# Kernel tuning notes

Measured on AMD Instinct MI355X. Metric: run time of the kernel, lower is better.

Reference implementation:

```python
import jax, jax.numpy as jnp
import numpy as np

DECAY = 0.99
EPS = 1e-5
NUM_EMBEDDINGS = 8192


def setup_inputs() -> dict:
    key = jax.random.key(0)
    k1, k2 = jax.random.split(key)
    N, D, K = 65536, 64, NUM_EMBEDDINGS
    x = jax.random.normal(k1, (N, D), dtype=jnp.float32)
    vq_embedding = jax.random.uniform(k2, (K, D), dtype=jnp.float32)
    vq_cluster_size = jnp.ones((K,), dtype=jnp.float32)
    return {"x": x, "vq_embedding": vq_embedding, "vq_cluster_size": vq_cluster_size}


def reference(x, vq_embedding, vq_cluster_size):
    N, D = x.shape
    K = vq_embedding.shape[0]

    # BatchNorm1d(affine=False), training mode: normalize with batch stats (biased var)
    mean = jnp.mean(x, axis=0)                      # [D]
    var = jnp.var(x, axis=0)                        # biased, [D]
    xn = (x - mean) / jnp.sqrt(var + EPS)           # [N, D]

    # pairwise squared distances [N, K]
    distances = (jnp.sum(xn * xn, axis=1, keepdims=True)
                 + jnp.sum(vq_embedding * vq_embedding, axis=1)
                 - 2.0 * (xn @ vq_embedding.T))
    idx = jnp.argmin(distances, axis=1)             # [N]

    # one-hot scatter expressed as segment sums
    dw = jax.ops.segment_sum(xn, idx, num_segments=K)                      # [K, D]
    counts = jax.ops.segment_sum(jnp.ones((N,), x.dtype), idx, num_segments=K)  # [K]

    # EMA codebook update
    new_emb = vq_cluster_size[:, None] * vq_embedding * DECAY + (1.0 - DECAY) * dw
    new_size = vq_cluster_size * DECAY + (1.0 - DECAY) * counts
    new_emb = new_emb / new_size[:, None]

    # BN running stats with momentum=None (cumulative avg, first batch):
    # running_mean = batch mean, running_var = unbiased batch var
    unbiased_var = var * (N / (N - 1))
    running_std = jnp.sqrt(unbiased_var + EPS)
    vq_embedding_output = new_emb * running_std[None, :] + mean[None, :]

    return vq_embedding_output, new_emb, new_size
```

## Files before the change

### kernel.cpp

```cpp
#include <hip/hip_runtime.h>

#define NROWS 65536
#define DIM 64
#define KCODES 8192
#define DECAYF 0.99f
#define EPSV 1e-5f
#define KD (KCODES * DIM)
#define KSPLIT 4
#define KC (KCODES / KSPLIT)
#define ROUNDS (KC / 128)

typedef _Float16 half8 __attribute__((ext_vector_type(8)));
typedef float f32x16 __attribute__((ext_vector_type(16)));

#define WS_STATS  0
#define WS_NHCK   256
#define WS_EBUF   8448
#define WS_PSUM   270592
#define WS_PSQ    286976
#define WS_PACKED 303360
#define WS_DW     368896
#define WS_COUNTS 893184
#define ZERO_F4   149504

__global__ __launch_bounds__(256) void k_prep_stats(
    const float* __restrict__ emb, const float* __restrict__ x,
    half8* __restrict__ ebuf, float* __restrict__ nhck,
    float* __restrict__ psum, float* __restrict__ psq,
    float4* __restrict__ zbase)
{
    const int tid = blockIdx.x * 256 + threadIdx.x;

    #pragma unroll
    for (int i = 0; i < 3; ++i) {
        int z = tid + i * 65536;
        if (z < ZERO_F4) zbase[z] = float4{0.f, 0.f, 0.f, 0.f};
    }

    {
        const int code = tid >> 3, sub = tid & 7;
        const int c = sub >> 1, h = sub & 1;
        const float* e = emb + (size_t)code * DIM + c * 16 + h * 8;
        float4 a = *(const float4*)e;
        float4 b = *(const float4*)(e + 4);
        float f[8] = {a.x, a.y, a.z, a.w, b.x, b.y, b.z, b.w};
        half8 hh;
        float ssq = 0.f;
        #pragma unroll
        for (int i = 0; i < 8; ++i) {
            hh[i] = (_Float16)(f[i] - 0.5f);
            ssq += f[i] * f[i];
        }
        #pragma unroll
        for (int o = 1; o < 8; o <<= 1) ssq += __shfl_xor(ssq, o, 64);
        if (sub == 0) nhck[code] = 10.6875f - 0.5f * ssq;
        const int R = code >> 7, t = (code >> 5) & 3, col = code & 31;
        ebuf[(size_t)R * 1024 + t * 256 + c * 64 + h * 32 + col] = hh;
    }

    {
        const int wave = threadIdx.x >> 6;
        const int col  = threadIdx.x & 63;
        const int base = blockIdx.x * 256;
        float s = 0.f, q = 0.f;
        #pragma unroll 4
        for (int i = 0; i < 64; ++i) {
            int r = base + i * 4 + wave;
            float v = x[(size_t)r * DIM + col];
            s += v;
            q += v * v;
        }
        __shared__ float ls[4][64];
        __shared__ float lq[4][64];
        ls[wave][col] = s;
        lq[wave][col] = q;
        __syncthreads();
        if (threadIdx.x < 64) {
            psum[blockIdx.x * 64 + col] = ls[0][col] + ls[1][col] + ls[2][col] + ls[3][col];
            psq[blockIdx.x * 64 + col]  = lq[0][col] + lq[1][col] + lq[2][col] + lq[3][col];
        }
    }
}

__global__ __launch_bounds__(256) void k_colstats_final(
    const float* __restrict__ psum, const float* __restrict__ psq,
    float* __restrict__ stats)
{
    const int col = threadIdx.x & 63, part = threadIdx.x >> 6;
    float s = 0.f, q = 0.f;
    for (int i = part * 64; i < part * 64 + 64; ++i) {
        s += psum[i * 64 + col];
        q += psq[i * 64 + col];
    }
    __shared__ float ls[4][64];
    __shared__ float lq[4][64];
    ls[part][col] = s;
    lq[part][col] = q;
    __syncthreads();
    if (threadIdx.x < 64) {
        s = ls[0][col] + ls[1][col] + ls[2][col] + ls[3][col];
        q = lq[0][col] + lq[1][col] + lq[2][col] + lq[3][col];
        const float n = (float)NROWS;
        float mean = s / n;
        float var = q / n - mean * mean;
        if (var < 0.f) var = 0.f;
        stats[col]       = mean;
        stats[64 + col]  = 1.0f / sqrtf(var + EPSV);
        stats[128 + col] = sqrtf(var * (n / (n - 1.0f)) + EPSV);
    }
}

__device__ __forceinline__ void gload16(const void* g, void* l)
{
    __builtin_amdgcn_global_load_lds(
        (const __attribute__((address_space(1))) void*)g,
        (__attribute__((address_space(3))) void*)l, 16, 0, 0);
}

__global__ __launch_bounds__(256) void k_argmin32(
    const float* __restrict__ x, const half8* __restrict__ ebuf,
    const float* __restrict__ nhckg, const float* __restrict__ stats,
    unsigned* __restrict__ packed)
{
    __shared__ half8 smem[2048];

    const int lane = threadIdx.x & 63;
    const int wave = threadIdx.x >> 6;
    const int kc = blockIdx.y;
    const int col = lane & 31, h = lane >> 5;
    const int myrow = blockIdx.x * 128 + wave * 32 + col;

    half8 ah[4];
    {
        const float* xr = x + (size_t)myrow * DIM + h * 8;
        #pragma unroll
        for (int c = 0; c < 4; ++c) {
            float4 v0  = *(const float4*)(xr + c * 16);
            float4 v1  = *(const float4*)(xr + c * 16 + 4);
            float4 mu0 = *(const float4*)(stats + h * 8 + c * 16);
            float4 mu1 = *(const float4*)(stats + h * 8 + c * 16 + 4);
            float4 sg0 = *(const float4*)(stats + 64 + h * 8 + c * 16);
            float4 sg1 = *(const float4*)(stats + 64 + h * 8 + c * 16 + 4);
            ah[c][0] = (_Float16)((v0.x - mu0.x) * sg0.x);
            ah[c][1] = (_Float16)((v0.y - mu0.y) * sg0.y);
            ah[c][2] = (_Float16)((v0.z - mu0.z) * sg0.z);
            ah[c][3] = (_Float16)((v0.w - mu0.w) * sg0.w);
            ah[c][4] = (_Float16)((v1.x - mu1.x) * sg1.x);
            ah[c][5] = (_Float16)((v1.y - mu1.y) * sg1.y);
            ah[c][6] = (_Float16)((v1.z - mu1.z) * sg1.z);
            ah[c][7] = (_Float16)((v1.w - mu1.w) * sg1.w);
        }
    }

    float best[16];
    #pragma unroll
    for (int i = 0; i < 16; ++i) best[i] = -3.4e38f;

    const half8* esrc = ebuf + (size_t)kc * (KC * 8);
    const float* ckb = nhckg + kc * KC;

    {
        const char* src = (const char*)esrc + threadIdx.x * 16;
        char* dst = (char*)smem + threadIdx.x * 16;
        #pragma unroll
        for (int i = 0; i < 4; ++i) gload16(src + i * 4096, dst + i * 4096);
    }
    float nhck[4];
    #pragma unroll
    for (int t = 0; t < 4; ++t) nhck[t] = ckb[t * 32 + col];
    __syncthreads();

    for (int R = 0; R < ROUNDS; ++R) {
        const int buf = R & 1;
        float nhck_n[4] = {0.f, 0.f, 0.f, 0.f};
        if (R < ROUNDS - 1) {
            const char* src = (const char*)esrc + (size_t)(R + 1) * 16384 + threadIdx.x * 16;
            char* dst = (char*)smem + (buf ^ 1) * 16384 + threadIdx.x * 16;
            #pragma unroll
            for (int i = 0; i < 4; ++i) gload16(src + i * 4096, dst + i * 4096);
            #pragma unroll
            for (int t = 0; t < 4; ++t) nhck_n[t] = ckb[(R + 1) * 128 + t * 32 + col];
        }

        const half8* sb = smem + buf * 1024 + lane;
        #pragma unroll
        for (int t = 0; t < 4; ++t) {
            half8 b0 = sb[t * 256];
            half8 b1 = sb[t * 256 + 64];
            half8 b2 = sb[t * 256 + 128];
            half8 b3 = sb[t * 256 + 192];
            f32x16 acc;
            #pragma unroll
            for (int i = 0; i < 16; ++i) acc[i] = nhck[t];
            __builtin_amdgcn_s_setprio(1);
            acc = __builtin_amdgcn_mfma_f32_32x32x16_f16(ah[0], b0, acc, 0, 0, 0);
            acc = __builtin_amdgcn_mfma_f32_32x32x16_f16(ah[1], b1, acc, 0, 0, 0);
            acc = __builtin_amdgcn_mfma_f32_32x32x16_f16(ah[2], b2, acc, 0, 0, 0);
            acc = __builtin_amdgcn_mfma_f32_32x32x16_f16(ah[3], b3, acc, 0, 0, 0);
            __builtin_amdgcn_s_setprio(0);
            const unsigned key =
                (unsigned)(8191 - (kc * KC + R * 128 + t * 32 + col)) & 0x1FFFu;
            #pragma unroll
            for (int i = 0; i < 16; ++i) {
                unsigned u = (__float_as_uint(acc[i]) & 0xFFFFE000u) | key;
                best[i] = fmaxf(best[i], __uint_as_float(u));
            }
        }
        __syncthreads();
        #pragma unroll
        for (int t = 0; t < 4; ++t) nhck[t] = nhck_n[t];
    }

    #pragma unroll
    for (int off = 1; off < 32; off <<= 1) {
        #pragma unroll
        for (int i = 0; i < 16; ++i)
            best[i] = fmaxf(best[i], __shfl_xor(best[i], off, 64));
    }
    if (col == 0) {
        const int rbase = blockIdx.x * 128 + wave * 32 + 4 * h;
        #pragma unroll
        for (int i = 0; i < 16; ++i) {
            int row = rbase + (i & 3) + 8 * (i >> 2);
            unsigned u = __float_as_uint(best[i]);
            u = (u & 0x80000000u) ? ~u : (u | 0x80000000u);
            atomicMax(&packed[row], u);
        }
    }
}

__global__ __launch_bounds__(256) void k_scatter(
    const float* __restrict__ x, const float* __restrict__ stats,
    const unsigned* __restrict__ packed,
    float* __restrict__ dw, float* __restrict__ counts)
{
    const int t = blockIdx.x * 256 + threadIdx.x;
    const int row = t >> 6, col = t & 63;
    const unsigned v = packed[row];
    const unsigned key = (v & 0x80000000u) ? (v & 8191u) : (~v & 8191u);
    const int j = 8191 - (int)key;
    float xv = (x[(size_t)row * DIM + col] - stats[col]) * stats[64 + col];
    atomicAdd(&dw[(size_t)j * DIM + col], xv);
    if (col == 0) atomicAdd(&counts[j], 1.0f);
}

__global__ __launch_bounds__(256) void k_final(
    const float* __restrict__ emb, const float* __restrict__ cs,
    const float* __restrict__ dw, const float* __restrict__ counts,
    const float* __restrict__ stats, float* __restrict__ out)
{
    const int t = blockIdx.x * 256 + threadIdx.x;
    const int k = t >> 6, d = t & 63;
    float csk = cs[k];
    float ns = csk * DECAYF + (1.f - DECAYF) * counts[k];
    float ne = (csk * emb[t] * DECAYF + (1.f - DECAYF) * dw[t]) / ns;
    out[KD + t] = ne;
    out[t] = ne * stats[128 + d] + stats[d];
    if (d == 0) out[2 * KD + k] = ns;
}

extern "C" void kernel_launch(void* const* d_in, const int* in_sizes, int n_in,
                              void* d_out, int out_size, void* d_ws, size_t ws_size,
                              hipStream_t stream)
{
    const float* x   = (const float*)d_in[0];
    const float* emb = (const float*)d_in[1];
    const float* cs  = (const float*)d_in[2];
    float* out = (float*)d_out;
    float* ws  = (float*)d_ws;

    float* stats  = ws + WS_STATS;
    float* nhck   = ws + WS_NHCK;
    half8* ebuf   = (half8*)(ws + WS_EBUF);
    float* psum   = ws + WS_PSUM;
    float* psq    = ws + WS_PSQ;
    unsigned* packed = (unsigned*)(ws + WS_PACKED);
    float* dw     = ws + WS_DW;
    float* counts = ws + WS_COUNTS;

    k_prep_stats<<<256, 256, 0, stream>>>(emb, x, ebuf, nhck, psum, psq,
                                          (float4*)(ws + WS_PACKED));
    k_colstats_final<<<1, 256, 0, stream>>>(psum, psq, stats);
    dim3 g3(NROWS / 128, KSPLIT);
    k_argmin32<<<g3, 256, 0, stream>>>(x, ebuf, nhck, stats, packed);
    k_scatter<<<(NROWS * DIM) / 256, 256, 0, stream>>>(x, stats, packed, dw, counts);
    k_final<<<KD / 256, 256, 0, stream>>>(emb, cs, dw, counts, stats, out);
}
```

Measured before the change: 175.2 us.

## Switch argmin GEMM to 16x16x32 MFMA with XOR-swizzled codebook layout

Replaces the 32x32x16 MFMA tiling in the distance/argmin kernel with 16x16x32 MFMAs. Each wave now handles 16 rows instead of 32, the grid doubles in rows, and the codebook is repacked in LDS with an XOR swizzle to avoid bank conflicts. This shrinks per-thread accumulator and best-value registers (16 down to 4), aiming for higher occupancy and a cheaper epilogue. In exchange, each row block rereads the codebook twice as often and more LDS loads are issued per MFMA.

```diff
diff --git a/kernel.cpp b/kernel.cpp
--- a/kernel.cpp
+++ b/kernel.cpp
@@ -11,7 +11,7 @@
 #define ROUNDS (KC / 128)
 
 typedef _Float16 half8 __attribute__((ext_vector_type(8)));
-typedef float f32x16 __attribute__((ext_vector_type(16)));
+typedef float f32x4 __attribute__((ext_vector_type(4)));
 
 #define WS_STATS  0
 #define WS_NHCK   256
@@ -38,9 +38,8 @@
     }
 
     {
-        const int code = tid >> 3, sub = tid & 7;
-        const int c = sub >> 1, h = sub & 1;
-        const float* e = emb + (size_t)code * DIM + c * 16 + h * 8;
+        const int code = tid >> 3, ch = tid & 7;
+        const float* e = emb + (size_t)code * DIM + ch * 8;
         float4 a = *(const float4*)e;
         float4 b = *(const float4*)(e + 4);
         float f[8] = {a.x, a.y, a.z, a.w, b.x, b.y, b.z, b.w};
@@ -53,9 +52,9 @@
         }
         #pragma unroll
         for (int o = 1; o < 8; o <<= 1) ssq += __shfl_xor(ssq, o, 64);
-        if (sub == 0) nhck[code] = 10.6875f - 0.5f * ssq;
-        const int R = code >> 7, t = (code >> 5) & 3, col = code & 31;
-        ebuf[(size_t)R * 1024 + t * 256 + c * 64 + h * 32 + col] = hh;
+        if (ch == 0) nhck[code] = 10.6875f - 0.5f * ssq;
+        const int c = code & 15;
+        ebuf[(size_t)(code >> 4) * 128 + c * 8 + (ch ^ (c & 7))] = hh;
     }
 
     {
@@ -117,7 +116,7 @@
         (__attribute__((address_space(3))) void*)l, 16, 0, 0);
 }
 
-__global__ __launch_bounds__(256) void k_argmin32(
+__global__ __launch_bounds__(256) void k_argmin16(
     const float* __restrict__ x, const half8* __restrict__ ebuf,
     const float* __restrict__ nhckg, const float* __restrict__ stats,
     unsigned* __restrict__ packed)
@@ -127,37 +126,52 @@
     const int lane = threadIdx.x & 63;
     const int wave = threadIdx.x >> 6;
     const int kc = blockIdx.y;
-    const int col = lane & 31, h = lane >> 5;
-    const int myrow = blockIdx.x * 128 + wave * 32 + col;
-
-    half8 ah[4];
-    {
-        const float* xr = x + (size_t)myrow * DIM + h * 8;
-        #pragma unroll
-        for (int c = 0; c < 4; ++c) {
-            float4 v0  = *(const float4*)(xr + c * 16);
-            float4 v1  = *(const float4*)(xr + c * 16 + 4);
-            float4 mu0 = *(const float4*)(stats + h * 8 + c * 16);
-            float4 mu1 = *(const float4*)(stats + h * 8 + c * 16 + 4);
-            float4 sg0 = *(const float4*)(stats + 64 + h * 8 + c * 16);
-            float4 sg1 = *(const float4*)(stats + 64 + h * 8 + c * 16 + 4);
-            ah[c][0] = (_Float16)((v0.x - mu0.x) * sg0.x);
-            ah[c][1] = (_Float16)((v0.y - mu0.y) * sg0.y);
-            ah[c][2] = (_Float16)((v0.z - mu0.z) * sg0.z);
-            ah[c][3] = (_Float16)((v0.w - mu0.w) * sg0.w);
-            ah[c][4] = (_Float16)((v1.x - mu1.x) * sg1.x);
-            ah[c][5] = (_Float16)((v1.y - mu1.y) * sg1.y);
-            ah[c][6] = (_Float16)((v1.z - mu1.z) * sg1.z);
-            ah[c][7] = (_Float16)((v1.w - mu1.w) * sg1.w);
-        }
-    }
-
-    float best[16];
-    #pragma unroll
-    for (int i = 0; i < 16; ++i) best[i] = -3.4e38f;
+    const int c  = lane & 15;
+    const int kg = lane >> 4;
+    const int rowbase = blockIdx.x * 64 + wave * 16;
+    const int myrow = rowbase + c;
+
+    half8 a0, a1;
+    {
+        const float* xr = x + (size_t)myrow * DIM;
+        const int d0 = kg * 8, d1 = 32 + kg * 8;
+        float4 v0 = *(const float4*)(xr + d0);
+        float4 v1 = *(const float4*)(xr + d0 + 4);
+        float4 w0 = *(const float4*)(xr + d1);
+        float4 w1 = *(const float4*)(xr + d1 + 4);
+        float4 m0 = *(const float4*)(stats + d0);
+        float4 m1 = *(const float4*)(stats + d0 + 4);
+        float4 n0 = *(const float4*)(stats + d1);
+        float4 n1 = *(const float4*)(stats + d1 + 4);
+        float4 s0 = *(const float4*)(stats + 64 + d0);
+        float4 s1 = *(const float4*)(stats + 64 + d0 + 4);
+        float4 t0 = *(const float4*)(stats + 64 + d1);
+        float4 t1 = *(const float4*)(stats + 64 + d1 + 4);
+        a0[0] = (_Float16)((v0.x - m0.x) * s0.x);
+        a0[1] = (_Float16)((v0.y - m0.y) * s0.y);
+        a0[2] = (_Float16)((v0.z - m0.z) * s0.z);
+        a0[3] = (_Float16)((v0.w - m0.w) * s0.w);
+        a0[4] = (_Float16)((v1.x - m1.x) * s1.x);
+        a0[5] = (_Float16)((v1.y - m1.y) * s1.y);
+        a0[6] = (_Float16)((v1.z - m1.z) * s1.z);
+        a0[7] = (_Float16)((v1.w - m1.w) * s1.w);
+        a1[0] = (_Float16)((w0.x - n0.x) * t0.x);
+        a1[1] = (_Float16)((w0.y - n0.y) * t0.y);
+        a1[2] = (_Float16)((w0.z - n0.z) * t0.z);
+        a1[3] = (_Float16)((w0.w - n0.w) * t0.w);
+        a1[4] = (_Float16)((w1.x - n1.x) * t1.x);
+        a1[5] = (_Float16)((w1.y - n1.y) * t1.y);
+        a1[6] = (_Float16)((w1.z - n1.z) * t1.z);
+        a1[7] = (_Float16)((w1.w - n1.w) * t1.w);
+    }
+
+    float best[4];
+    #pragma unroll
+    for (int i = 0; i < 4; ++i) best[i] = -3.4e38f;
 
     const half8* esrc = ebuf + (size_t)kc * (KC * 8);
     const float* ckb = nhckg + kc * KC;
+    const unsigned kbase = (unsigned)(8191 - kc * KC - c);
 
     {
         const char* src = (const char*)esrc + threadIdx.x * 16;
@@ -165,63 +179,58 @@
         #pragma unroll
         for (int i = 0; i < 4; ++i) gload16(src + i * 4096, dst + i * 4096);
     }
-    float nhck[4];
-    #pragma unroll
-    for (int t = 0; t < 4; ++t) nhck[t] = ckb[t * 32 + col];
+    float nv[8];
+    #pragma unroll
+    for (int t = 0; t < 8; ++t) nv[t] = ckb[t * 16 + c];
     __syncthreads();
 
     for (int R = 0; R < ROUNDS; ++R) {
         const int buf = R & 1;
-        float nhck_n[4] = {0.f, 0.f, 0.f, 0.f};
+        float nvn[8] = {0.f, 0.f, 0.f, 0.f, 0.f, 0.f, 0.f, 0.f};
         if (R < ROUNDS - 1) {
             const char* src = (const char*)esrc + (size_t)(R + 1) * 16384 + threadIdx.x * 16;
             char* dst = (char*)smem + (buf ^ 1) * 16384 + threadIdx.x * 16;
             #pragma unroll
             for (int i = 0; i < 4; ++i) gload16(src + i * 4096, dst + i * 4096);
             #pragma unroll
-            for (int t = 0; t < 4; ++t) nhck_n[t] = ckb[(R + 1) * 128 + t * 32 + col];
-        }
-
-        const half8* sb = smem + buf * 1024 + lane;
-        #pragma unroll
-        for (int t = 0; t < 4; ++t) {
-            half8 b0 = sb[t * 256];
-            half8 b1 = sb[t * 256 + 64];
-            half8 b2 = sb[t * 256 + 128];
-            half8 b3 = sb[t * 256 + 192];
-            f32x16 acc;
-            #pragma unroll
-            for (int i = 0; i < 16; ++i) acc[i] = nhck[t];
+            for (int t = 0; t < 8; ++t) nvn[t] = ckb[(R + 1) * 128 + t * 16 + c];
+        }
+
+        const unsigned kR = kbase - (unsigned)(R * 128);
+        const half8* sb = smem + buf * 1024 + c * 8;
+        #pragma unroll
+        for (int t = 0; t < 8; ++t) {
+            half8 b0 = sb[t * 128 + (kg ^ (c & 7))];
+            half8 b1 = sb[t * 128 + ((kg + 4) ^ (c & 7))];
+            f32x4 acc;
+            #pragma unroll
+            for (int i = 0; i < 4; ++i) acc[i] = nv[t];
             __builtin_amdgcn_s_setprio(1);
-            acc = __builtin_amdgcn_mfma_f32_32x32x16_f16(ah[0], b0, acc, 0, 0, 0);
-            acc = __builtin_amdgcn_mfma_f32_32x32x16_f16(ah[1], b1, acc, 0, 0, 0);
-            acc = __builtin_amdgcn_mfma_f32_32x32x16_f16(ah[2], b2, acc, 0, 0, 0);
-            acc = __builtin_amdgcn_mfma_f32_32x32x16_f16(ah[3], b3, acc, 0, 0, 0);
+            acc = __builtin_amdgcn_mfma_f32_16x16x32_f16(a0, b0, acc, 0, 0, 0);
+            acc = __builtin_amdgcn_mfma_f32_16x16x32_f16(a1, b1, acc, 0, 0, 0);
             __builtin_amdgcn_s_setprio(0);
-            const unsigned key =
-                (unsigned)(8191 - (kc * KC + R * 128 + t * 32 + col)) & 0x1FFFu;
-            #pragma unroll
-            for (int i = 0; i < 16; ++i) {
+            const unsigned key = kR - (unsigned)(t * 16);
+            #pragma unroll
+            for (int i = 0; i < 4; ++i) {
                 unsigned u = (__float_as_uint(acc[i]) & 0xFFFFE000u) | key;
                 best[i] = fmaxf(best[i], __uint_as_float(u));
             }
         }
         __syncthreads();
         #pragma unroll
-        for (int t = 0; t < 4; ++t) nhck[t] = nhck_n[t];
-    }
-
-    #pragma unroll
-    for (int off = 1; off < 32; off <<= 1) {
-        #pragma unroll
-        for (int i = 0; i < 16; ++i)
+        for (int t = 0; t < 8; ++t) nv[t] = nvn[t];
+    }
+
+    #pragma unroll
+    for (int off = 1; off < 16; off <<= 1) {
+        #pragma unroll
+        for (int i = 0; i < 4; ++i)
             best[i] = fmaxf(best[i], __shfl_xor(best[i], off, 64));
     }
-    if (col == 0) {
-        const int rbase = blockIdx.x * 128 + wave * 32 + 4 * h;
-        #pragma unroll
-        for (int i = 0; i < 16; ++i) {
-            int row = rbase + (i & 3) + 8 * (i >> 2);
+    if (c == 0) {
+        #pragma unroll
+        for (int i = 0; i < 4; ++i) {
+            int row = rowbase + kg * 4 + i;
             unsigned u = __float_as_uint(best[i]);
             u = (u & 0x80000000u) ? ~u : (u | 0x80000000u);
             atomicMax(&packed[row], u);
@@ -281,8 +290,8 @@
     k_prep_stats<<<256, 256, 0, stream>>>(emb, x, ebuf, nhck, psum, psq,
                                           (float4*)(ws + WS_PACKED));
     k_colstats_final<<<1, 256, 0, stream>>>(psum, psq, stats);
-    dim3 g3(NROWS / 128, KSPLIT);
-    k_argmin32<<<g3, 256, 0, stream>>>(x, ebuf, nhck, stats, packed);
+    dim3 g3(NROWS / 64, KSPLIT);
+    k_argmin16<<<g3, 256, 0, stream>>>(x, ebuf, nhck, stats, packed);
     k_scatter<<<(NROWS * DIM) / 256, 256, 0, stream>>>(x, stats, packed, dw, counts);
     k_final<<<KD / 256, 256, 0, stream>>>(emb, cs, dw, counts, stats, out);
 }
```

After: 170.9 us. 2.5% less time.

## Process two 32-row A tiles per wave to reuse codebook fragments

Applied to the files above, without the earlier changes.

Each wave now handles 64 rows instead of 32, keeping two A-fragment sets and two accumulators so every B fragment read from LDS feeds two MFMA chains. The grid is halved in the row dimension. This halves the codebook LDS traffic and global staging per row and interleaves independent MFMAs to hide their latency. The cost is higher register pressure and fewer blocks (1024 total), which could lower occupancy.

```diff
diff --git a/kernel.cpp b/kernel.cpp
--- a/kernel.cpp
+++ b/kernel.cpp
@@ -117,6 +117,30 @@
         (__attribute__((address_space(3))) void*)l, 16, 0, 0);
 }
 
+__device__ __forceinline__ void build_afrag(const float* __restrict__ xr,
+                                            const float* __restrict__ stats,
+                                            int h, half8* a)
+{
+    #pragma unroll
+    for (int c = 0; c < 4; ++c) {
+        const int d = c * 16 + h * 8;
+        float4 v0 = *(const float4*)(xr + d);
+        float4 v1 = *(const float4*)(xr + d + 4);
+        float4 m0 = *(const float4*)(stats + d);
+        float4 m1 = *(const float4*)(stats + d + 4);
+        float4 s0 = *(const float4*)(stats + 64 + d);
+        float4 s1 = *(const float4*)(stats + 64 + d + 4);
+        a[c][0] = (_Float16)((v0.x - m0.x) * s0.x);
+        a[c][1] = (_Float16)((v0.y - m0.y) * s0.y);
+        a[c][2] = (_Float16)((v0.z - m0.z) * s0.z);
+        a[c][3] = (_Float16)((v0.w - m0.w) * s0.w);
+        a[c][4] = (_Float16)((v1.x - m1.x) * s1.x);
+        a[c][5] = (_Float16)((v1.y - m1.y) * s1.y);
+        a[c][6] = (_Float16)((v1.z - m1.z) * s1.z);
+        a[c][7] = (_Float16)((v1.w - m1.w) * s1.w);
+    }
+}
+
 __global__ __launch_bounds__(256) void k_argmin32(
     const float* __restrict__ x, const half8* __restrict__ ebuf,
     const float* __restrict__ nhckg, const float* __restrict__ stats,
@@ -128,33 +152,15 @@
     const int wave = threadIdx.x >> 6;
     const int kc = blockIdx.y;
     const int col = lane & 31, h = lane >> 5;
-    const int myrow = blockIdx.x * 128 + wave * 32 + col;
-
-    half8 ah[4];
-    {
-        const float* xr = x + (size_t)myrow * DIM + h * 8;
-        #pragma unroll
-        for (int c = 0; c < 4; ++c) {
-            float4 v0  = *(const float4*)(xr + c * 16);
-            float4 v1  = *(const float4*)(xr + c * 16 + 4);
-            float4 mu0 = *(const float4*)(stats + h * 8 + c * 16);
-            float4 mu1 = *(const float4*)(stats + h * 8 + c * 16 + 4);
-            float4 sg0 = *(const float4*)(stats + 64 + h * 8 + c * 16);
-            float4 sg1 = *(const float4*)(stats + 64 + h * 8 + c * 16 + 4);
-            ah[c][0] = (_Float16)((v0.x - mu0.x) * sg0.x);
-            ah[c][1] = (_Float16)((v0.y - mu0.y) * sg0.y);
-            ah[c][2] = (_Float16)((v0.z - mu0.z) * sg0.z);
-            ah[c][3] = (_Float16)((v0.w - mu0.w) * sg0.w);
-            ah[c][4] = (_Float16)((v1.x - mu1.x) * sg1.x);
-            ah[c][5] = (_Float16)((v1.y - mu1.y) * sg1.y);
-            ah[c][6] = (_Float16)((v1.z - mu1.z) * sg1.z);
-            ah[c][7] = (_Float16)((v1.w - mu1.w) * sg1.w);
-        }
-    }
-
-    float best[16];
-    #pragma unroll
-    for (int i = 0; i < 16; ++i) best[i] = -3.4e38f;
+    const int rowbase = blockIdx.x * 256 + wave * 64;
+
+    half8 a0[4], a1[4];
+    build_afrag(x + (size_t)(rowbase + col) * DIM, stats, h, a0);
+    build_afrag(x + (size_t)(rowbase + 32 + col) * DIM, stats, h, a1);
+
+    float best0[16], best1[16];
+    #pragma unroll
+    for (int i = 0; i < 16; ++i) { best0[i] = -3.4e38f; best1[i] = -3.4e38f; }
 
     const half8* esrc = ebuf + (size_t)kc * (KC * 8);
     const float* ckb = nhckg + kc * KC;
@@ -165,21 +171,21 @@
         #pragma unroll
         for (int i = 0; i < 4; ++i) gload16(src + i * 4096, dst + i * 4096);
     }
-    float nhck[4];
-    #pragma unroll
-    for (int t = 0; t < 4; ++t) nhck[t] = ckb[t * 32 + col];
+    float nv[4];
+    #pragma unroll
+    for (int t = 0; t < 4; ++t) nv[t] = ckb[t * 32 + col];
     __syncthreads();
 
     for (int R = 0; R < ROUNDS; ++R) {
         const int buf = R & 1;
-        float nhck_n[4] = {0.f, 0.f, 0.f, 0.f};
+        float nvn[4] = {0.f, 0.f, 0.f, 0.f};
         if (R < ROUNDS - 1) {
             const char* src = (const char*)esrc + (size_t)(R + 1) * 16384 + threadIdx.x * 16;
             char* dst = (char*)smem + (buf ^ 1) * 16384 + threadIdx.x * 16;
             #pragma unroll
             for (int i = 0; i < 4; ++i) gload16(src + i * 4096, dst + i * 4096);
             #pragma unroll
-            for (int t = 0; t < 4; ++t) nhck_n[t] = ckb[(R + 1) * 128 + t * 32 + col];
+            for (int t = 0; t < 4; ++t) nvn[t] = ckb[(R + 1) * 128 + t * 32 + col];
         }
 
         const half8* sb = smem + buf * 1024 + lane;
@@ -189,42 +195,52 @@
             half8 b1 = sb[t * 256 + 64];
             half8 b2 = sb[t * 256 + 128];
             half8 b3 = sb[t * 256 + 192];
-            f32x16 acc;
+            f32x16 acc0, acc1;
             #pragma unroll
-            for (int i = 0; i < 16; ++i) acc[i] = nhck[t];
+            for (int i = 0; i < 16; ++i) { acc0[i] = nv[t]; acc1[i] = nv[t]; }
             __builtin_amdgcn_s_setprio(1);
-            acc = __builtin_amdgcn_mfma_f32_32x32x16_f16(ah[0], b0, acc, 0, 0, 0);
-            acc = __builtin_amdgcn_mfma_f32_32x32x16_f16(ah[1], b1, acc, 0, 0, 0);
-            acc = __builtin_amdgcn_mfma_f32_32x32x16_f16(ah[2], b2, acc, 0, 0, 0);
-            acc = __builtin_amdgcn_mfma_f32_32x32x16_f16(ah[3], b3, acc, 0, 0, 0);
+            acc0 = __builtin_amdgcn_mfma_f32_32x32x16_f16(a0[0], b0, acc0, 0, 0, 0);
+            acc1 = __builtin_amdgcn_mfma_f32_32x32x16_f16(a1[0], b0, acc1, 0, 0, 0);
+            acc0 = __builtin_amdgcn_mfma_f32_32x32x16_f16(a0[1], b1, acc0, 0, 0, 0);
+            acc1 = __builtin_amdgcn_mfma_f32_32x32x16_f16(a1[1], b1, acc1, 0, 0, 0);
+            acc0 = __builtin_amdgcn_mfma_f32_32x32x16_f16(a0[2], b2, acc0, 0, 0, 0);
+            acc1 = __builtin_amdgcn_mfma_f32_32x32x16_f16(a1[2], b2, acc1, 0, 0, 0);
+            acc0 = __builtin_amdgcn_mfma_f32_32x32x16_f16(a0[3], b3, acc0, 0, 0, 0);
+            acc1 = __builtin_amdgcn_mfma_f32_32x32x16_f16(a1[3], b3, acc1, 0, 0, 0);
             __builtin_amdgcn_s_setprio(0);
-            const unsigned key =
-                (unsigned)(8191 - (kc * KC + R * 128 + t * 32 + col)) & 0x1FFFu;
+            const unsigned key = (unsigned)(8191 - (kc * KC + R * 128 + t * 32 + col));
             #pragma unroll
             for (int i = 0; i < 16; ++i) {
-                unsigned u = (__float_as_uint(acc[i]) & 0xFFFFE000u) | key;
-                best[i] = fmaxf(best[i], __uint_as_float(u));
+                unsigned u0 = (__float_as_uint(acc0[i]) & 0xFFFFE000u) | key;
+                best0[i] = fmaxf(best0[i], __uint_as_float(u0));
+                unsigned u1 = (__float_as_uint(acc1[i]) & 0xFFFFE000u) | key;
+                best1[i] = fmaxf(best1[i], __uint_as_float(u1));
             }
         }
         __syncthreads();
         #pragma unroll
-        for (int t = 0; t < 4; ++t) nhck[t] = nhck_n[t];
+        for (int t = 0; t < 4; ++t) nv[t] = nvn[t];
     }
 
     #pragma unroll
     for (int off = 1; off < 32; off <<= 1) {
         #pragma unroll
-        for (int i = 0; i < 16; ++i)
-            best[i] = fmaxf(best[i], __shfl_xor(best[i], off, 64));
+        for (int i = 0; i < 16; ++i) {
+            best0[i] = fmaxf(best0[i], __shfl_xor(best0[i], off, 64));
+            best1[i] = fmaxf(best1[i], __shfl_xor(best1[i], off, 64));
+        }
     }
     if (col == 0) {
-        const int rbase = blockIdx.x * 128 + wave * 32 + 4 * h;
+        const int rb = rowbase + 4 * h;
         #pragma unroll
         for (int i = 0; i < 16; ++i) {
-            int row = rbase + (i & 3) + 8 * (i >> 2);
-            unsigned u = __float_as_uint(best[i]);
-            u = (u & 0x80000000u) ? ~u : (u | 0x80000000u);
-            atomicMax(&packed[row], u);
+            int row = rb + (i & 3) + 8 * (i >> 2);
+            unsigned u0 = __float_as_uint(best0[i]);
+            u0 = (u0 & 0x80000000u) ? ~u0 : (u0 | 0x80000000u);
+            atomicMax(&packed[row], u0);
+            unsigned u1 = __float_as_uint(best1[i]);
+            u1 = (u1 & 0x80000000u) ? ~u1 : (u1 | 0x80000000u);
+            atomicMax(&packed[row + 32], u1);
         }
     }
 }
@@ -281,7 +297,7 @@
     k_prep_stats<<<256, 256, 0, stream>>>(emb, x, ebuf, nhck, psum, psq,
                                           (float4*)(ws + WS_PACKED));
     k_colstats_final<<<1, 256, 0, stream>>>(psum, psq, stats);
-    dim3 g3(NROWS / 128, KSPLIT);
+    dim3 g3(NROWS / 256, KSPLIT);
     k_argmin32<<<g3, 256, 0, stream>>>(x, ebuf, nhck, stats, packed);
     k_scatter<<<(NROWS * DIM) / 256, 256, 0, stream>>>(x, stats, packed, dw, counts);
     k_final<<<KD / 256, 256, 0, stream>>>(emb, cs, dw, counts, stats, out);
```

Result: faster. 157.1 us (-10.3%).
